# Kernel optimization log

Hardware: AMD Instinct MI355X
Metric: run time of the kernel (lower is better)

## Reference

```python
import jax, jax.numpy as jnp
import numpy as np
from jax import lax

B, CIN, COUT, H, W, K = 256, 512, 256, 8, 8, 8192


def setup_inputs() -> dict:
    key = jax.random.key(0)
    ks = jax.random.split(key, 6)
    scale = 0.05
    return {
        "latent": jax.random.normal(ks[0], (B, CIN, H, W), dtype=jnp.float32),
        "conv_w": jax.random.normal(ks[1], (COUT, CIN, 3, 3), dtype=jnp.float32) * scale,
        "conv_b": jax.random.normal(ks[2], (COUT,), dtype=jnp.float32) * scale,
        "lin_w": jax.random.normal(ks[3], (COUT, COUT), dtype=jnp.float32) * scale,
        "lin_b": jax.random.normal(ks[4], (COUT,), dtype=jnp.float32) * scale,
        "emb": jax.random.normal(ks[5], (K, COUT), dtype=jnp.float32),
    }


def reference(latent, conv_w, conv_b, lin_w, lin_b, emb):
    # pre-quantization conv: 3x3, stride 1, padding 1 (SAME), NCHW / OIHW
    x = lax.conv_general_dilated(
        latent, conv_w, window_strides=(1, 1), padding="SAME",
        dimension_numbers=("NCHW", "OIHW", "NCHW"),
    ) + conv_b[None, :, None, None]
    # permute(0,2,3,1) then linear on last dim
    x = jnp.transpose(x, (0, 2, 3, 1))              # [B,H,W,C]
    x = jnp.einsum("bhwc,dc->bhwd", x, lin_w) + lin_b
    flat = x.reshape(-1, x.shape[-1])               # [B*H*W, C]
    distances = (
        jnp.sum(flat ** 2, axis=1, keepdims=True)
        + jnp.sum(emb ** 2, axis=1)
        - 2.0 * flat @ emb.T
    )                                               # [B*H*W, K]
    encoding_indices = jnp.argmin(distances, axis=1)
    return encoding_indices.reshape(-1, 64)
```

## Files before the change

### kernel.cpp

```cpp
#include <hip/hip_runtime.h>
#include <cstdint>
#include <cstddef>


#define CIN_  512
#define E_    4608
#define M_    16384

typedef _Float16 half4_t __attribute__((ext_vector_type(4)));
typedef _Float16 half8_t __attribute__((ext_vector_type(8)));
typedef float f32x4 __attribute__((ext_vector_type(4)));

#define GLOAD_LDS16(gptr, lptr)                                         \
    __builtin_amdgcn_global_load_lds(                                   \
        (const __attribute__((address_space(1))) unsigned int*)(gptr),  \
        (__attribute__((address_space(3))) unsigned int*)(lptr), 16, 0, 0)

__global__ void tkern(const float* __restrict__ src, float* __restrict__ dst,
                      int R, int C) {
    __shared__ float t[32][33];
    int c = blockIdx.x * 32 + threadIdx.x;
    int r = blockIdx.y * 32 + threadIdx.y;
    if (r < R && c < C) t[threadIdx.y][threadIdx.x] = src[(size_t)r * C + c];
    __syncthreads();
    int rr = blockIdx.x * 32 + threadIdx.y;
    int cc = blockIdx.y * 32 + threadIdx.x;
    if (rr < C && cc < R) dst[(size_t)rr * R + cc] = t[threadIdx.x][threadIdx.y];
}

__global__ __launch_bounds__(256) void fold5_k(const float* __restrict__ conv_w,
                                               const float* __restrict__ lwT,
                                               _Float16* __restrict__ W2x) {
    int e0 = blockIdx.x * 8;
    int d = threadIdx.x;
    float acc[8];
    #pragma unroll
    for (int j = 0; j < 8; ++j) acc[j] = 0.f;
    for (int co = 0; co < 256; ++co) {
        float lw = lwT[co * 256 + d];
        const float* cwr = conv_w + (size_t)co * E_ + e0;
        #pragma unroll
        for (int j = 0; j < 8; ++j) acc[j] += cwr[j] * lw;
    }
    #pragma unroll
    for (int j = 0; j < 8; ++j) {
        int e = e0 + j;
        int c = e / 9, t9 = e - c * 9;
        _Float16 h = (_Float16)acc[j];
        _Float16 l = (_Float16)(acc[j] - (float)h);
        W2x[((size_t)(t9 * 256 + d)) * 512 + c] = h;
        W2x[((size_t)((9 + t9) * 256 + d)) * 512 + c] = l;
    }
}

__global__ void bias_k(const float* __restrict__ lwT, const float* __restrict__ conv_b,
                       const float* __restrict__ lin_b, float* __restrict__ b2) {
    int d = threadIdx.x;
    float acc = lin_b[d];
    for (int co = 0; co < 256; ++co) acc += lwT[co * 256 + d] * conv_b[co];
    b2[d] = acc;
}

__global__ __launch_bounds__(256) void packlat_k(const float* __restrict__ lat,
                                                 _Float16* __restrict__ Xnp) {
    int b = blockIdx.x, t = threadIdx.x;
    __shared__ float lt[128][65];
    const float* src = lat + (size_t)b * 512 * 64;
    _Float16* dst = Xnp + (size_t)b * 64 * 1024;
    for (int c0 = 0; c0 < 512; c0 += 128) {
        __syncthreads();
        #pragma unroll
        for (int j = 0; j < 8; ++j) {
            int f4 = t + j * 256;
            int cc = f4 >> 4, p4 = (f4 & 15) * 4;
            float4 v = *(const float4*)(src + (size_t)(c0 + cc) * 64 + p4);
            lt[cc][p4] = v.x; lt[cc][p4 + 1] = v.y;
            lt[cc][p4 + 2] = v.z; lt[cc][p4 + 3] = v.w;
        }
        __syncthreads();
        int pix = t >> 2, cr = (t & 3) * 32;
        #pragma unroll
        for (int q = 0; q < 4; ++q) {
            half8_t hh, ll;
            #pragma unroll
            for (int j = 0; j < 8; ++j) {
                float v = lt[cr + q * 8 + j][pix];
                _Float16 h = (_Float16)v;
                hh[j] = h; ll[j] = (_Float16)(v - (float)h);
            }
            *(half8_t*)(dst + (size_t)pix * 1024 + c0 + cr + q * 8) = hh;
            *(half8_t*)(dst + (size_t)pix * 1024 + 512 + c0 + cr + q * 8) = ll;
        }
    }
}

__global__ __launch_bounds__(256) void convm6_k(
    const _Float16* __restrict__ Xnp, const _Float16* __restrict__ W2x,
    const float* __restrict__ b2, float* __restrict__ yb) {
    __shared__ char sm[65536];
    int m0 = blockIdx.x * 128, n0 = blockIdx.y * 128;
    int tid = threadIdx.x, w = tid >> 6, lane = tid & 63;
    int wm = w & 1, wn = w >> 1;
    int fr = lane & 15, fq = lane >> 4;

    int xq = (fq ^ ((fr >> 1) & 3)) << 4;
    int boff[4];
    #pragma unroll
    for (int i = 0; i < 4; ++i) boff[i] = (wn * 64 + i * 16 + fr) * 64 + xq;
    int imgoff[4], ph[4], pw[4];
    #pragma unroll
    for (int s = 0; s < 4; ++s) {
        int rr = wm * 64 + s * 16 + fr;
        imgoff[s] = rr & 64; ph[s] = (rr >> 3) & 7; pw[s] = rr & 7;
    }
    int slt[2], sr[2], sq[2];
    #pragma unroll
    for (int i = 0; i < 2; ++i) {
        int s = w * 128 + i * 64 + lane;
        slt[i] = s;
        sr[i] = s >> 2;
        sq[i] = ((s & 3) ^ ((s >> 3) & 3)) * 8;
    }

    auto stageA = [&](int cc, int buf) {
        char* L = sm + buf * 16384;
        #pragma unroll
        for (int i = 0; i < 2; ++i) {
            const _Float16* base =
                Xnp + (size_t)(m0 + sr[i]) * 1024 + cc * 32 + sq[i];
            GLOAD_LDS16(base, L + slt[i] * 16);
            GLOAD_LDS16(base + 512, L + 8192 + slt[i] * 16);
        }
    };
    auto stageB = [&](int tap, int cc, int buf) {
        char* L = sm + 32768 + buf * 16384;
        #pragma unroll
        for (int i = 0; i < 2; ++i) {
            const _Float16* bb =
                W2x + ((size_t)(tap * 256 + n0 + sr[i])) * 512 + cc * 32 + sq[i];
            GLOAD_LDS16(bb, L + slt[i] * 16);
            GLOAD_LDS16(bb + (size_t)9 * 256 * 512, L + 8192 + slt[i] * 16);
        }
    };

    f32x4 acc[4][4];
    #pragma unroll
    for (int s = 0; s < 4; ++s)
        #pragma unroll
        for (int t = 0; t < 4; ++t)
            #pragma unroll
            for (int r = 0; r < 4; ++r) acc[s][t][r] = 0.f;

    stageA(0, 0);
    stageB(0, 0, 0);
    const half8_t zfrag = {};
    int gi = 0;
    for (int cc = 0; cc < 16; ++cc) {
        const char* Ab = sm + (cc & 1) * 16384;
        for (int tap = 0; tap < 9; ++tap, ++gi) {
            __syncthreads();
            if (tap < 8) stageB(tap + 1, cc, (gi + 1) & 1);
            else if (cc < 15) stageB(0, cc + 1, (gi + 1) & 1);
            if (tap == 7 && cc < 15) stageA(cc + 1, (cc + 1) & 1);

            int dy = tap / 3 - 1, dx = tap - (tap / 3) * 3 - 1;
            half8_t ah[4], al[4];
            #pragma unroll
            for (int s = 0; s < 4; ++s) {
                int ih = ph[s] + dy, iw = pw[s] + dx;
                bool v = ((unsigned)ih < 8u) && ((unsigned)iw < 8u);
                int pp = imgoff[s] + (v ? ih * 8 + iw : 0);
                int ao = pp * 64 + ((fq ^ ((pp >> 1) & 3)) << 4);
                half8_t a0 = *(const half8_t*)(Ab + ao);
                half8_t a1 = *(const half8_t*)(Ab + 8192 + ao);
                ah[s] = v ? a0 : zfrag;
                al[s] = v ? a1 : zfrag;
            }
            const char* Bb = sm + 32768 + (gi & 1) * 16384;
            half8_t bh[4], bl[4];
            #pragma unroll
            for (int t = 0; t < 4; ++t) {
                bh[t] = *(const half8_t*)(Bb + boff[t]);
                bl[t] = *(const half8_t*)(Bb + 8192 + boff[t]);
            }
            #pragma unroll
            for (int s = 0; s < 4; ++s)
                #pragma unroll
                for (int t = 0; t < 4; ++t)
                    acc[s][t] = __builtin_amdgcn_mfma_f32_16x16x32_f16(
                        ah[s], bh[t], acc[s][t], 0, 0, 0);
            #pragma unroll
            for (int s = 0; s < 4; ++s)
                #pragma unroll
                for (int t = 0; t < 4; ++t)
                    acc[s][t] = __builtin_amdgcn_mfma_f32_16x16x32_f16(
                        ah[s], bl[t], acc[s][t], 0, 0, 0);
            #pragma unroll
            for (int s = 0; s < 4; ++s)
                #pragma unroll
                for (int t = 0; t < 4; ++t)
                    acc[s][t] = __builtin_amdgcn_mfma_f32_16x16x32_f16(
                        al[s], bh[t], acc[s][t], 0, 0, 0);
        }
    }

    float bv[4];
    #pragma unroll
    for (int t = 0; t < 4; ++t) bv[t] = b2[n0 + wn * 64 + t * 16 + fr];
    #pragma unroll
    for (int s = 0; s < 4; ++s)
        #pragma unroll
        for (int r = 0; r < 4; ++r) {
            int m = m0 + wm * 64 + s * 16 + fq * 4 + r;
            #pragma unroll
            for (int t = 0; t < 4; ++t) {
                int d = n0 + wn * 64 + t * 16 + fr;
                yb[(size_t)m * 256 + d] = acc[s][t][r] + bv[t];
            }
        }
}

__global__ __launch_bounds__(256) void pack2_k(
    const float* __restrict__ yb, const float* __restrict__ emb,
    _Float16* __restrict__ A2, _Float16* __restrict__ B2,
    float* __restrict__ esq) {
    #pragma unroll
    for (int it = 0; it < 8; ++it) {
        int i = (blockIdx.x + it * 512) * 256 + threadIdx.x;
        float4 v = *(const float4*)(yb + (size_t)i * 4);
        half4_t h = {(_Float16)v.x, (_Float16)v.y, (_Float16)v.z, (_Float16)v.w};
        *(half4_t*)(A2 + (size_t)i * 4) = h;
    }
    int w = threadIdx.x >> 6, lane = threadIdx.x & 63;
    #pragma unroll
    for (int j = 0; j < 4; ++j) {
        int k = blockIdx.x * 16 + w * 4 + j;
        float4 v = *(const float4*)(emb + (size_t)k * 256 + lane * 4);
        half4_t h = {(_Float16)v.x, (_Float16)v.y, (_Float16)v.z, (_Float16)v.w};
        *(half4_t*)(B2 + (size_t)k * 256 + lane * 4) = h;
        float s = v.x * v.x + v.y * v.y + v.z * v.z + v.w * v.w;
        #pragma unroll
        for (int m = 32; m >= 1; m >>= 1) s += __shfl_xor(s, m, 64);
        if (lane == 0) esq[k] = s;
    }
}

__global__ __launch_bounds__(256) void screen7_k(
    const _Float16* __restrict__ A2, const _Float16* __restrict__ B2,
    const float* __restrict__ esq, float* __restrict__ ps2, int* __restrict__ pi2) {
    __shared__ char sm[32768];
    int Lb = blockIdx.x;
    int xcd = Lb & 7, j = Lb >> 3;
    int mt = xcd * 16 + (j & 15);
    int nt = j >> 4;
    int m0 = mt * 128, n0 = nt * 128;
    int tid = threadIdx.x, w = tid >> 6, lane = tid & 63;
    int wm = w & 1, wn = w >> 1;
    int fr = lane & 15, fq = lane >> 4;

    int xq = (fq ^ ((fr >> 1) & 3)) << 4;
    int aoff[4], boff[4];
    #pragma unroll
    for (int i = 0; i < 4; ++i) {
        aoff[i] = (wm * 64 + i * 16 + fr) * 64 + xq;
        boff[i] = (wn * 64 + i * 16 + fr) * 64 + xq;
    }
    int slt[2], sr[2], sq[2];
    #pragma unroll
    for (int i = 0; i < 2; ++i) {
        int s = w * 128 + i * 64 + lane;
        slt[i] = s;
        sr[i] = s >> 2;
        sq[i] = ((s & 3) ^ ((s >> 3) & 3)) * 8;
    }

    auto stage = [&](int kt, int buf) {
        char* L = sm + buf * 16384;
        int ko = kt * 32;
        #pragma unroll
        for (int i = 0; i < 2; ++i) {
            GLOAD_LDS16(A2 + (size_t)(m0 + sr[i]) * 256 + ko + sq[i],
                        L + slt[i] * 16);
            GLOAD_LDS16(B2 + (size_t)(n0 + sr[i]) * 256 + ko + sq[i],
                        L + 8192 + slt[i] * 16);
        }
    };

    f32x4 acc[4][4];
    #pragma unroll
    for (int s = 0; s < 4; ++s)
        #pragma unroll
        for (int t = 0; t < 4; ++t)
            #pragma unroll
            for (int r = 0; r < 4; ++r) acc[s][t][r] = 0.f;

    stage(0, 0);
    for (int kt = 0; kt < 8; ++kt) {
        __syncthreads();
        if (kt + 1 < 8) stage(kt + 1, (kt + 1) & 1);
        const char* L = sm + (kt & 1) * 16384;
        half8_t af[4], bf[4];
        #pragma unroll
        for (int s = 0; s < 4; ++s) af[s] = *(const half8_t*)(L + aoff[s]);
        #pragma unroll
        for (int t = 0; t < 4; ++t) bf[t] = *(const half8_t*)(L + 8192 + boff[t]);
        #pragma unroll
        for (int s = 0; s < 4; ++s)
            #pragma unroll
            for (int t = 0; t < 4; ++t)
                acc[s][t] = __builtin_amdgcn_mfma_f32_16x16x32_f16(
                    af[s], bf[t], acc[s][t], 0, 0, 0);
    }

    float esv[4];
    #pragma unroll
    for (int t = 0; t < 4; ++t) esv[t] = esq[n0 + wn * 64 + t * 16 + fr];
    int colIdx = nt * 2 + wn;
    #pragma unroll
    for (int s = 0; s < 4; ++s) {
        #pragma unroll
        for (int r = 0; r < 4; ++r) {
            float best = 3.4e38f; int bidx = 0x7fffffff;
            #pragma unroll
            for (int t = 0; t < 4; ++t) {
                float sc = esv[t] - 2.f * acc[s][t][r];
                int k = n0 + wn * 64 + t * 16 + fr;
                if (sc < best || (sc == best && k < bidx)) { best = sc; bidx = k; }
            }
            #pragma unroll
            for (int msk = 1; msk <= 8; msk <<= 1) {
                float so = __shfl_xor(best, msk, 64);
                int ko2 = __shfl_xor(bidx, msk, 64);
                if (so < best || (so == best && ko2 < bidx)) { best = so; bidx = ko2; }
            }
            if (fr == 0) {
                int m = m0 + wm * 64 + s * 16 + fq * 4 + r;
                ps2[(size_t)m * 128 + colIdx] = best;
                pi2[(size_t)m * 128 + colIdx] = bidx;
            }
        }
    }
}

__global__ __launch_bounds__(256) void refine3_k(
    const float* __restrict__ y, const float* __restrict__ emb,
    const float* __restrict__ esq, const float* __restrict__ ps2,
    const int* __restrict__ pi2, int* __restrict__ out) {
    int lane = threadIdx.x & 63;
    for (int j = 0; j < 8; ++j) {
        int m = blockIdx.x * 32 + j * 4 + (threadIdx.x >> 6);
        float4 yv = *(const float4*)(y + (size_t)m * 256 + lane * 4);
        float sc_[2]; int kc_[2];
        #pragma unroll
        for (int i = 0; i < 2; ++i) {
            sc_[i] = ps2[(size_t)m * 128 + lane * 2 + i];
            kc_[i] = pi2[(size_t)m * 128 + lane * 2 + i];
        }
        float s0 = fminf(sc_[0], sc_[1]);
        #pragma unroll
        for (int msk = 1; msk <= 32; msk <<= 1) s0 = fminf(s0, __shfl_xor(s0, msk, 64));
        float thr = s0 + 0.25f;
        float best = 3.4e38f; int bk = 0x7fffffff;
        for (int c = 0; c < 128; ++c) {
            float scc = __shfl(sc_[c & 1], c >> 1, 64);
            if (scc <= thr) {
                int k = __shfl(kc_[c & 1], c >> 1, 64);
                float4 ev = *(const float4*)(emb + (size_t)k * 256 + lane * 4);
                float d = yv.x * ev.x + yv.y * ev.y + yv.z * ev.z + yv.w * ev.w;
                #pragma unroll
                for (int msk = 1; msk <= 32; msk <<= 1) d += __shfl_xor(d, msk, 64);
                float sx = esq[k] - 2.f * d;
                if (sx < best || (sx == best && k < bk)) { best = sx; bk = k; }
            }
        }
        if (lane == 0) out[m] = bk;
    }
}

extern "C" void kernel_launch(void* const* d_in, const int* in_sizes, int n_in,
                              void* d_out, int out_size, void* d_ws, size_t ws_size,
                              hipStream_t stream) {
    const float* latent = (const float*)d_in[0];
    const float* conv_w = (const float*)d_in[1];
    const float* conv_b = (const float*)d_in[2];
    const float* lin_w  = (const float*)d_in[3];
    const float* lin_b  = (const float*)d_in[4];
    const float* emb    = (const float*)d_in[5];
    int* out = (int*)d_out;

    char* W = (char*)d_ws;
    float*    lwT = (float*)(W + 0);
    float*    b2  = (float*)(W + 262144);
    float*    esq = (float*)(W + 263168);
    float*    yb  = (float*)(W + 295936);
    _Float16* W2x = (_Float16*)(W + 17073152);
    _Float16* Xnp = (_Float16*)(W + 21792768);
    _Float16* A2  = (_Float16*)(W + 21792768);
    _Float16* B2  = (_Float16*)(W + 30181376);
    float*    ps2 = (float*)(W + 34375680);
    int*      pi2 = (int*)(W + 42764288);

    dim3 t32(32, 32);
    tkern<<<dim3(8, 8), t32, 0, stream>>>(lin_w, lwT, 256, 256);
    bias_k<<<1, 256, 0, stream>>>(lwT, conv_b, lin_b, b2);
    fold5_k<<<576, 256, 0, stream>>>(conv_w, lwT, W2x);
    packlat_k<<<256, 256, 0, stream>>>(latent, Xnp);

    convm6_k<<<dim3(128, 2), 256, 0, stream>>>(Xnp, W2x, b2, yb);

    pack2_k<<<512, 256, 0, stream>>>(yb, emb, A2, B2, esq);
    screen7_k<<<8192, 256, 0, stream>>>(A2, B2, esq, ps2, pi2);
    refine3_k<<<512, 256, 0, stream>>>(yb, emb, esq, ps2, pi2, out);
}
```

Measured before the change: 472.8 us.

## Make screen kernel persistent per 64-row tile, keep A resident, stream codebook

The distance screening kernel now launches one 512-thread block per 64 rows of activations. It loads the whole 64x256 A tile into LDS once and streams all 8192 codebook rows through a double-buffered B stage, 512 columns per outer step. The goal is to cut the A reloads and the per-block launch and prologue cost of the old 8192 small blocks. In exchange only 256 blocks run, using 96KB of LDS each, so occupancy and latency hiding are lower and each block has a long serial loop.

```diff
diff --git a/kernel.cpp b/kernel.cpp
--- a/kernel.cpp
+++ b/kernel.cpp
@@ -245,46 +245,48 @@
     }
 }
 
-__global__ __launch_bounds__(256) void screen7_k(
+__global__ __launch_bounds__(512) void screen8_k(
     const _Float16* __restrict__ A2, const _Float16* __restrict__ B2,
     const float* __restrict__ esq, float* __restrict__ ps2, int* __restrict__ pi2) {
-    __shared__ char sm[32768];
-    int Lb = blockIdx.x;
-    int xcd = Lb & 7, j = Lb >> 3;
-    int mt = xcd * 16 + (j & 15);
-    int nt = j >> 4;
-    int m0 = mt * 128, n0 = nt * 128;
+    __shared__ char sm[98304];
+    int m0 = blockIdx.x * 64;
     int tid = threadIdx.x, w = tid >> 6, lane = tid & 63;
-    int wm = w & 1, wn = w >> 1;
     int fr = lane & 15, fq = lane >> 4;
-
     int xq = (fq ^ ((fr >> 1) & 3)) << 4;
+
     int aoff[4], boff[4];
     #pragma unroll
     for (int i = 0; i < 4; ++i) {
-        aoff[i] = (wm * 64 + i * 16 + fr) * 64 + xq;
-        boff[i] = (wn * 64 + i * 16 + fr) * 64 + xq;
-    }
-    int slt[2], sr[2], sq[2];
-    #pragma unroll
-    for (int i = 0; i < 2; ++i) {
-        int s = w * 128 + i * 64 + lane;
-        slt[i] = s;
-        sr[i] = s >> 2;
-        sq[i] = ((s & 3) ^ ((s >> 3) & 3)) * 8;
-    }
-
-    auto stage = [&](int kt, int buf) {
-        char* L = sm + buf * 16384;
-        int ko = kt * 32;
-        #pragma unroll
-        for (int i = 0; i < 2; ++i) {
-            GLOAD_LDS16(A2 + (size_t)(m0 + sr[i]) * 256 + ko + sq[i],
-                        L + slt[i] * 16);
-            GLOAD_LDS16(B2 + (size_t)(n0 + sr[i]) * 256 + ko + sq[i],
-                        L + 8192 + slt[i] * 16);
+        aoff[i] = (i * 16 + fr) * 64 + xq;
+        boff[i] = (w * 64 + i * 16 + fr) * 64 + xq;
+    }
+
+    int gA_row[4], gA_ch[4], gB_row[4], gSq[4];
+    #pragma unroll
+    for (int i = 0; i < 4; ++i) {
+        int g = i * 512 + tid;
+        gA_row[i] = (g >> 2) & 63;
+        gA_ch[i]  = g >> 8;
+        gB_row[i] = g >> 2;
+        gSq[i]    = ((g & 3) ^ ((g >> 3) & 3)) * 8;
+    }
+
+    #pragma unroll
+    for (int i = 0; i < 4; ++i) {
+        int g = i * 512 + tid;
+        GLOAD_LDS16(A2 + (size_t)(m0 + gA_row[i]) * 256 + gA_ch[i] * 32 + gSq[i],
+                    sm + g * 16);
+    }
+    auto stageB = [&](int n0, int ko, int buf) {
+        char* L = sm + 32768 + buf * 32768;
+        #pragma unroll
+        for (int i = 0; i < 4; ++i) {
+            int g = i * 512 + tid;
+            GLOAD_LDS16(B2 + (size_t)(n0 + gB_row[i]) * 256 + ko + gSq[i],
+                        L + g * 16);
         }
     };
+    stageB(0, 0, 0);
 
     f32x4 acc[4][4];
     #pragma unroll
@@ -294,51 +296,61 @@
             #pragma unroll
             for (int r = 0; r < 4; ++r) acc[s][t][r] = 0.f;
 
-    stage(0, 0);
-    for (int kt = 0; kt < 8; ++kt) {
-        __syncthreads();
-        if (kt + 1 < 8) stage(kt + 1, (kt + 1) & 1);
-        const char* L = sm + (kt & 1) * 16384;
-        half8_t af[4], bf[4];
-        #pragma unroll
-        for (int s = 0; s < 4; ++s) af[s] = *(const half8_t*)(L + aoff[s]);
-        #pragma unroll
-        for (int t = 0; t < 4; ++t) bf[t] = *(const half8_t*)(L + 8192 + boff[t]);
+    int gi = 0;
+    for (int nt = 0; nt < 16; ++nt) {
+        int n0 = nt * 512;
+        for (int kt = 0; kt < 8; ++kt, ++gi) {
+            __syncthreads();
+            if (kt < 7)       stageB(n0, (kt + 1) * 32, (gi + 1) & 1);
+            else if (nt < 15) stageB(n0 + 512, 0, (gi + 1) & 1);
+            const char* Ab = sm + kt * 4096;
+            const char* Bb = sm + 32768 + (gi & 1) * 32768;
+            half8_t af[4], bf[4];
+            #pragma unroll
+            for (int s = 0; s < 4; ++s) af[s] = *(const half8_t*)(Ab + aoff[s]);
+            #pragma unroll
+            for (int t = 0; t < 4; ++t) bf[t] = *(const half8_t*)(Bb + boff[t]);
+            #pragma unroll
+            for (int s = 0; s < 4; ++s)
+                #pragma unroll
+                for (int t = 0; t < 4; ++t)
+                    acc[s][t] = __builtin_amdgcn_mfma_f32_16x16x32_f16(
+                        af[s], bf[t], acc[s][t], 0, 0, 0);
+        }
+        float esv[4];
+        #pragma unroll
+        for (int t = 0; t < 4; ++t) esv[t] = esq[n0 + w * 64 + t * 16 + fr];
+        int colIdx = nt * 8 + w;
+        #pragma unroll
+        for (int s = 0; s < 4; ++s) {
+            #pragma unroll
+            for (int r = 0; r < 4; ++r) {
+                float best = 3.4e38f; int bidx = 0x7fffffff;
+                #pragma unroll
+                for (int t = 0; t < 4; ++t) {
+                    float sc = esv[t] - 2.f * acc[s][t][r];
+                    int k = n0 + w * 64 + t * 16 + fr;
+                    if (sc < best || (sc == best && k < bidx)) { best = sc; bidx = k; }
+                }
+                #pragma unroll
+                for (int msk = 1; msk <= 8; msk <<= 1) {
+                    float so = __shfl_xor(best, msk, 64);
+                    int ko2 = __shfl_xor(bidx, msk, 64);
+                    if (so < best || (so == best && ko2 < bidx)) { best = so; bidx = ko2; }
+                }
+                if (fr == 0) {
+                    int m = m0 + s * 16 + fq * 4 + r;
+                    ps2[(size_t)m * 128 + colIdx] = best;
+                    pi2[(size_t)m * 128 + colIdx] = bidx;
+                }
+            }
+        }
         #pragma unroll
         for (int s = 0; s < 4; ++s)
             #pragma unroll
             for (int t = 0; t < 4; ++t)
-                acc[s][t] = __builtin_amdgcn_mfma_f32_16x16x32_f16(
-                    af[s], bf[t], acc[s][t], 0, 0, 0);
-    }
-
-    float esv[4];
-    #pragma unroll
-    for (int t = 0; t < 4; ++t) esv[t] = esq[n0 + wn * 64 + t * 16 + fr];
-    int colIdx = nt * 2 + wn;
-    #pragma unroll
-    for (int s = 0; s < 4; ++s) {
-        #pragma unroll
-        for (int r = 0; r < 4; ++r) {
-            float best = 3.4e38f; int bidx = 0x7fffffff;
-            #pragma unroll
-            for (int t = 0; t < 4; ++t) {
-                float sc = esv[t] - 2.f * acc[s][t][r];
-                int k = n0 + wn * 64 + t * 16 + fr;
-                if (sc < best || (sc == best && k < bidx)) { best = sc; bidx = k; }
-            }
-            #pragma unroll
-            for (int msk = 1; msk <= 8; msk <<= 1) {
-                float so = __shfl_xor(best, msk, 64);
-                int ko2 = __shfl_xor(bidx, msk, 64);
-                if (so < best || (so == best && ko2 < bidx)) { best = so; bidx = ko2; }
-            }
-            if (fr == 0) {
-                int m = m0 + wm * 64 + s * 16 + fq * 4 + r;
-                ps2[(size_t)m * 128 + colIdx] = best;
-                pi2[(size_t)m * 128 + colIdx] = bidx;
-            }
-        }
+                #pragma unroll
+                for (int r = 0; r < 4; ++r) acc[s][t][r] = 0.f;
     }
 }
 
@@ -409,6 +421,6 @@
     convm6_k<<<dim3(128, 2), 256, 0, stream>>>(Xnp, W2x, b2, yb);
 
     pack2_k<<<512, 256, 0, stream>>>(yb, emb, A2, B2, esq);
-    screen7_k<<<8192, 256, 0, stream>>>(A2, B2, esq, ps2, pi2);
+    screen8_k<<<256, 512, 0, stream>>>(A2, B2, esq, ps2, pi2);
     refine3_k<<<512, 256, 0, stream>>>(yb, emb, esq, ps2, pi2, out);
 }
```

After: 555.4 us. +17.5%, slower.
